# Kernel optimization log

Hardware: AMD Instinct MI355X
Metric: run time of the kernel (lower is better)

## Reference

```python
import jax, jax.numpy as jnp
import numpy as np

B, S, D, H = 64, 256, 2048, 16
HD = D // H

def setup_inputs() -> dict:
    key = jax.random.key(0)
    k1, k2, k3 = jax.random.split(key, 3)
    x = jax.random.normal(k1, (B, S, D), dtype=jnp.float32)
    # torch Linear weights: [out_features, in_features], scaled like kaiming-ish init
    w_qkv = jax.random.normal(k2, (3 * D, D), dtype=jnp.float32) * (1.0 / np.sqrt(D))
    w_o = jax.random.normal(k3, (D, D), dtype=jnp.float32) * (1.0 / np.sqrt(D))
    return {"x": x, "w_qkv": w_qkv, "w_o": w_o}

def reference(x, w_qkv, w_o):
    b, s, d = x.shape
    qkv = jnp.einsum('bsd,ed->bse', x, w_qkv)            # [B,S,3D]
    qkv = qkv.reshape(b, s, 3, H, HD).transpose(2, 0, 3, 1, 4)  # [3,B,H,S,HD]
    q, k, v = qkv[0], qkv[1], qkv[2]
    scores = jnp.einsum('bhqd,bhkd->bhqk', q, k) * (HD ** -0.5)  # [B,H,S,S]
    causal = jnp.triu(jnp.ones((s, s), dtype=bool), 1)
    scores = jnp.where(causal, jnp.float32(-1e9), scores)
    a = jax.nn.softmax(scores, axis=-1)
    ctx = jnp.einsum('bhqk,bhkd->bhqd', a, v)            # [B,H,S,HD]
    ctx = ctx.transpose(0, 2, 1, 3).reshape(b, s, d)     # [B,S,D]
    return jnp.einsum('bsd,ed->bse', ctx, w_o)
```

## Files before the change

kernel.cpp:

```cpp
#include <hip/hip_runtime.h>

#define NB 64
#define NS 256
#define ND 2048
#define NH 16
#define NHD 128

typedef unsigned short ushort_t;
typedef __attribute__((ext_vector_type(8))) __bf16 bf16x8;
typedef __attribute__((ext_vector_type(4))) short shortx4;
typedef __attribute__((ext_vector_type(4))) float f32x4;
typedef __attribute__((ext_vector_type(4))) unsigned short ushortx4;

__device__ __forceinline__ unsigned short f2bf(float f) {
  union { float f; unsigned int u; } v; v.f = f;
  unsigned int r = v.u + 0x7FFFu + ((v.u >> 16) & 1u);
  return (unsigned short)(r >> 16);
}

__device__ __forceinline__ void gload16(const void* g, void* l) {
  __builtin_amdgcn_global_load_lds(
      (__attribute__((address_space(1))) void*)(void*)(g),
      (__attribute__((address_space(3))) void*)(l), 16, 0, 0);
}

__global__ void cast_f32_bf16(const float* __restrict__ in, ushort_t* __restrict__ out, long n) {
  long i = ((long)blockIdx.x * blockDim.x + threadIdx.x) * 4;
  if (i + 3 < n) {
    float4 v = *reinterpret_cast<const float4*>(in + i);
    ushortx4 o;
    o.x = f2bf(v.x); o.y = f2bf(v.y); o.z = f2bf(v.z); o.w = f2bf(v.w);
    *reinterpret_cast<ushortx4*>(out + i) = o;
  }
}

template<int MODE>
__global__ __launch_bounds__(512, 2) void gemm256(const ushort_t* __restrict__ A,
                                                  const ushort_t* __restrict__ Bt,
                                                  float* __restrict__ Cf,
                                                  ushort_t* __restrict__ Cq,
                                                  int M, int N, int K) {
  extern __shared__ char smem[];
  const int tid = threadIdx.x;
  const int wv = tid >> 6, lane = tid & 63;
  const int l15 = lane & 15, lg = lane >> 4;
  const int wm = wv >> 2, wn = wv & 3;

  const int nbn = N >> 8;
  const int nwg = (M >> 8) * nbn;
  const int bid = blockIdx.x;
  const int q8 = nwg >> 3, r8 = nwg & 7;
  const int xcd = bid & 7, lin = bid >> 3;
  const int wg = (xcd < r8 ? xcd * (q8 + 1) : r8 * (q8 + 1) + (xcd - r8) * q8) + lin;
  const int m0 = (wg / nbn) << 8;
  const int n0 = (wg % nbn) << 8;

  const int srow = wv * 16 + (lane >> 2);
  const int sce = ((lane & 3) * 8) ^ (((srow >> 1) & 3) << 3);
  const ushort_t* pa0 = A  + (long)(m0 + srow) * K + sce;
  const ushort_t* pa1 = pa0 + (long)128 * K;
  const ushort_t* pb0 = Bt + (long)(n0 + srow) * K + sce;
  const ushort_t* pb1 = pb0 + (long)128 * K;

  const int c = (lg * 16) ^ (((l15 >> 1) & 3) << 4);

  f32x4 acc[8][4] = {};
  const int nkt = K >> 5;

  bf16x8 faA[8], faB[4], fbA[8], fbB[4];

  #pragma unroll
  for (int tt = 0; tt < 3; ++tt) {
    char* d = smem + tt * 32768 + wv * 1024;
    const long ko = (long)tt * 32;
    gload16(pa0 + ko, d);
    gload16(pa1 + ko, d + 8192);
    gload16(pb0 + ko, d + 16384);
    gload16(pb1 + ko, d + 24576);
  }
  asm volatile("s_waitcnt vmcnt(8)" ::: "memory");
  __builtin_amdgcn_s_barrier();
  __builtin_amdgcn_sched_barrier(0);
  #pragma unroll
  for (int i = 0; i < 8; ++i)
    faA[i] = *reinterpret_cast<const bf16x8*>(smem + (wm * 128 + i * 16 + l15) * 64 + c);
  #pragma unroll
  for (int j = 0; j < 4; ++j)
    faB[j] = *reinterpret_cast<const bf16x8*>(smem + 16384 + (wn * 64 + j * 16 + l15) * 64 + c);
  asm volatile("s_waitcnt vmcnt(4)" ::: "memory");

#define TILE(T_, CA_, CB_, NA_, NB_)                                           \
  {                                                                            \
    const int t_ = (T_);                                                       \
    __builtin_amdgcn_s_barrier();                                              \
    asm volatile("s_waitcnt lgkmcnt(0)" ::: "memory");                         \
    __builtin_amdgcn_sched_barrier(0);                                         \
    __builtin_amdgcn_s_setprio(1);                                             \
    if (t_ + 1 < nkt) {                                                        \
      const char* rb = smem + ((t_ + 1) & 3) * 32768;                          \
      _Pragma("unroll")                                                        \
      for (int i = 0; i < 8; ++i)                                              \
        NA_[i] = *reinterpret_cast<const bf16x8*>(rb + (wm * 128 + i * 16 + l15) * 64 + c); \
      _Pragma("unroll")                                                        \
      for (int j = 0; j < 4; ++j)                                              \
        NB_[j] = *reinterpret_cast<const bf16x8*>(rb + 16384 + (wn * 64 + j * 16 + l15) * 64 + c); \
    }                                                                          \
    if (t_ + 3 < nkt) {                                                        \
      char* d = smem + ((t_ + 3) & 3) * 32768 + wv * 1024;                     \
      const long ko = (long)(t_ + 3) * 32;                                     \
      gload16(pa0 + ko, d);                                                    \
      gload16(pa1 + ko, d + 8192);                                             \
      gload16(pb0 + ko, d + 16384);                                            \
      gload16(pb1 + ko, d + 24576);                                            \
    }                                                                          \
    _Pragma("unroll")                                                          \
    for (int i = 0; i < 8; ++i)                                                \
      _Pragma("unroll")                                                        \
      for (int j = 0; j < 4; ++j)                                              \
        acc[i][j] = __builtin_amdgcn_mfma_f32_16x16x32_bf16(CA_[i], CB_[j], acc[i][j], 0, 0, 0); \
              \
    _Pragma("unroll")                                                          \
    for (int g = 0; g < 8; ++g) {                                              \
      __builtin_amdgcn_sched_group_barrier(0x008, 4, 0);                       \
      if (g < 6) __builtin_amdgcn_sched_group_barrier(0x100, 2, 0);            \
      if (g < 4) __builtin_amdgcn_sched_group_barrier(0x010, 1, 0);            \
    }                                                                          \
    __builtin_amdgcn_s_setprio(0);                                             \
    __builtin_amdgcn_sched_barrier(0);                                         \
    if (t_ + 3 < nkt) asm volatile("s_waitcnt vmcnt(4)" ::: "memory");         \
    else              asm volatile("s_waitcnt vmcnt(0)" ::: "memory");         \
  }

  for (int t = 0; t < nkt; t += 2) {
    TILE(t,     faA, faB, fbA, fbB);
    TILE(t + 1, fbA, fbB, faA, faB);
  }
#undef TILE

  #pragma unroll
  for (int k = 0; k < 8; ++k) {
    const int mrow = m0 + wm * 128 + k * 16 + lg * 4;
    #pragma unroll
    for (int j = 0; j < 4; ++j) {
      const int n = n0 + wn * 64 + j * 16 + l15;
      #pragma unroll
      for (int r = 0; r < 4; ++r) {
        const int m = mrow + r;
        const float v = acc[k][j][r];
        if (MODE == 0) {
          Cf[(long)m * N + n] = v;
        } else {
          const int tq = n >> 11, hh = (n >> 7) & 15, hd = n & 127;
          const int b = m >> 8, s = m & 255;
          Cq[((((long)tq * NB + b) * NH + hh) * NS + s) * NHD + hd] = f2bf(v);
        }
      }
    }
  }
}

__global__ __launch_bounds__(512) void attn_fused(const ushort_t* __restrict__ qkv,
                                                  ushort_t* __restrict__ ctx) {
  const int bh = blockIdx.x;
  const int b = bh >> 4, h = bh & 15;
  const int wave = threadIdx.x >> 6, lane = threadIdx.x & 63;
  const int l15 = lane & 15, lg = lane >> 4;
  const long head_off = ((long)(b * NH + h)) * (NS * NHD);
  const ushort_t* Qp = qkv + head_off;
  const ushort_t* Kp = qkv + (long)NB * NH * NS * NHD + head_off;
  const ushort_t* Vp = qkv + 2L * NB * NH * NS * NHD + head_off;
  const int q0 = wave * 32;

  bf16x8 qf[2][4];
  #pragma unroll
  for (int ni = 0; ni < 2; ++ni)
    #pragma unroll
    for (int kk = 0; kk < 4; ++kk)
      qf[ni][kk] = *reinterpret_cast<const bf16x8*>(Qp + (q0 + ni * 16 + l15) * NHD + kk * 32 + lg * 8);

  f32x4 o[8][2] = {};
  float mstate[2] = {-1e30f, -1e30f};
  float lstate[2] = {0.f, 0.f};
  const float scale = 0.08838834764831845f;
  const int ntiles = (q0 + 32 + 63) >> 6;

  for (int kt = 0; kt < ntiles; ++kt) {
    f32x4 st[4][2] = {};
    #pragma unroll
    for (int kk = 0; kk < 4; ++kk) {
      bf16x8 kf[4];
      #pragma unroll
      for (int mi = 0; mi < 4; ++mi)
        kf[mi] = *reinterpret_cast<const bf16x8*>(Kp + (kt * 64 + mi * 16 + l15) * NHD + kk * 32 + lg * 8);
      #pragma unroll
      for (int mi = 0; mi < 4; ++mi)
        #pragma unroll
        for (int ni = 0; ni < 2; ++ni)
          st[mi][ni] = __builtin_amdgcn_mfma_f32_16x16x32_bf16(kf[mi], qf[ni][kk], st[mi][ni], 0, 0, 0);
    }
    const bool last = (kt == ntiles - 1);
    #pragma unroll
    for (int mi = 0; mi < 4; ++mi)
      #pragma unroll
      for (int ni = 0; ni < 2; ++ni)
        #pragma unroll
        for (int r = 0; r < 4; ++r) {
          const int kc = kt * 64 + mi * 16 + lg * 4 + r;
          const int q = q0 + ni * 16 + l15;
          float v = st[mi][ni][r] * scale;
          if (last && kc > q) v = -1e30f;
          st[mi][ni][r] = v;
        }
    shortx4 p[4][2];
    #pragma unroll
    for (int ni = 0; ni < 2; ++ni) {
      float tmax = -1e30f;
      #pragma unroll
      for (int mi = 0; mi < 4; ++mi)
        #pragma unroll
        for (int r = 0; r < 4; ++r) tmax = fmaxf(tmax, st[mi][ni][r]);
      tmax = fmaxf(tmax, __shfl_xor(tmax, 16, 64));
      tmax = fmaxf(tmax, __shfl_xor(tmax, 32, 64));
      const float mnew = fmaxf(mstate[ni], tmax);
      const float alpha = __expf(mstate[ni] - mnew);
      float tsum = 0.f;
      #pragma unroll
      for (int mi = 0; mi < 4; ++mi)
        #pragma unroll
        for (int r = 0; r < 4; ++r) {
          const float pe = __expf(st[mi][ni][r] - mnew);
          st[mi][ni][r] = pe;
          tsum += pe;
        }
      tsum += __shfl_xor(tsum, 16, 64);
      tsum += __shfl_xor(tsum, 32, 64);
      lstate[ni] = lstate[ni] * alpha + tsum;
      mstate[ni] = mnew;
      #pragma unroll
      for (int f = 0; f < 8; ++f)
        #pragma unroll
        for (int r = 0; r < 4; ++r) o[f][ni][r] *= alpha;
      #pragma unroll
      for (int mi = 0; mi < 4; ++mi)
        #pragma unroll
        for (int r = 0; r < 4; ++r) p[mi][ni][r] = (short)f2bf(st[mi][ni][r]);
    }
    #pragma unroll
    for (int f = 0; f < 8; ++f)
      #pragma unroll
      for (int mi = 0; mi < 4; ++mi) {
        shortx4 vt;
        #pragma unroll
        for (int j = 0; j < 4; ++j)
          vt[j] = (short)Vp[(kt * 64 + mi * 16 + lg * 4 + j) * NHD + f * 16 + l15];
        #pragma unroll
        for (int ni = 0; ni < 2; ++ni)
          o[f][ni] = __builtin_amdgcn_mfma_f32_16x16x16bf16_1k(vt, p[mi][ni], o[f][ni], 0, 0, 0);
      }
  }
  const float inv0 = 1.f / lstate[0], inv1 = 1.f / lstate[1];
  #pragma unroll
  for (int f = 0; f < 8; ++f)
    #pragma unroll
    for (int ni = 0; ni < 2; ++ni) {
      const float inv = ni ? inv1 : inv0;
      const int q = q0 + ni * 16 + l15;
      const int hd = f * 16 + lg * 4;
      ushortx4 ov;
      #pragma unroll
      for (int r = 0; r < 4; ++r) ov[r] = f2bf(o[f][ni][r] * inv);
      *reinterpret_cast<ushortx4*>(ctx + ((long)(b * NS + q)) * ND + h * NHD + hd) = ov;
    }
}

extern "C" void kernel_launch(void* const* d_in, const int* in_sizes, int n_in,
                              void* d_out, int out_size, void* d_ws, size_t ws_size,
                              hipStream_t stream) {
  const float* x     = (const float*)d_in[0];
  const float* w_qkv = (const float*)d_in[1];
  const float* w_o   = (const float*)d_in[2];
  char* ws = (char*)d_ws;
  if (ws_size < 369098752UL) return;
  ushort_t* xb    = (ushort_t*)(ws);
  ushort_t* wqkvb = (ushort_t*)(ws + 67108864L);
  ushort_t* wob   = (ushort_t*)(ws + 92274688L);
  ushort_t* qkvb  = (ushort_t*)(ws + 100663296L);
  ushort_t* ctxb  = (ushort_t*)(ws + 301989888L);

  const long nx = (long)NB * NS * ND;
  const long nq = 3L * ND * ND;
  const long no = (long)ND * ND;
  cast_f32_bf16<<<dim3(nx / 1024), 256, 0, stream>>>(x, xb, nx);
  cast_f32_bf16<<<dim3(nq / 1024), 256, 0, stream>>>(w_qkv, wqkvb, nq);
  cast_f32_bf16<<<dim3(no / 1024), 256, 0, stream>>>(w_o, wob, no);

  const int lds_bytes = 4 * 32768;
  (void)hipFuncSetAttribute(reinterpret_cast<const void*>(&gemm256<1>),
                            hipFuncAttributeMaxDynamicSharedMemorySize, lds_bytes);
  (void)hipFuncSetAttribute(reinterpret_cast<const void*>(&gemm256<0>),
                            hipFuncAttributeMaxDynamicSharedMemorySize, lds_bytes);

  gemm256<1><<<dim3(64 * 24), 512, lds_bytes, stream>>>(xb, wqkvb, nullptr, qkvb,
                                                        NB * NS, 3 * ND, ND);
  attn_fused<<<dim3(NB * NH), 512, 0, stream>>>(qkvb, ctxb);
  gemm256<0><<<dim3(64 * 8), 512, lds_bytes, stream>>>(ctxb, wob, (float*)d_out, nullptr,
                                                       NB * NS, ND, ND);
}
```

Baseline: 705.8 us.

## Pre-transpose V and balance causal query blocks across waves

Adds a kernel that transposes V per head into [hd][s] layout, reusing the x bf16 buffer, so the PV MFMA operand becomes one vector load instead of four scattered scalar loads. The attention kernel also pairs each wave's 16 early query rows with 16 late rows, which balances causal work across waves and skips MFMAs for the early block once it is fully masked. The cost is an extra launch and a full read and write pass over V.

```diff
diff --git a/kernel.cpp b/kernel.cpp
--- a/kernel.cpp
+++ b/kernel.cpp
@@ -32,6 +32,19 @@
     o.x = f2bf(v.x); o.y = f2bf(v.y); o.z = f2bf(v.z); o.w = f2bf(v.w);
     *reinterpret_cast<ushortx4*>(out + i) = o;
   }
+}
+
+__global__ void transpose_v(const ushort_t* __restrict__ qkv_v, ushort_t* __restrict__ vt) {
+  const int g = blockIdx.x * 256 + threadIdx.x;
+  const int s = g & 255;
+  const int hd8 = (g >> 8) & 15;
+  const int bh = g >> 12;
+  const ushort_t* src = qkv_v + ((long)bh << 15) + s * 128 + hd8 * 8;
+  ushortx4 v0 = *reinterpret_cast<const ushortx4*>(src);
+  ushortx4 v1 = *reinterpret_cast<const ushortx4*>(src + 4);
+  ushort_t* dst = vt + ((long)bh << 15) + (long)(hd8 * 8) * 256 + s;
+  dst[0] = v0.x; dst[256] = v0.y; dst[512] = v0.z; dst[768] = v0.w;
+  dst[1024] = v1.x; dst[1280] = v1.y; dst[1536] = v1.z; dst[1792] = v1.w;
 }
 
 template<int MODE>
@@ -118,7 +131,6 @@
       _Pragma("unroll")                                                        \
       for (int j = 0; j < 4; ++j)                                              \
         acc[i][j] = __builtin_amdgcn_mfma_f32_16x16x32_bf16(CA_[i], CB_[j], acc[i][j], 0, 0, 0); \
-              \
     _Pragma("unroll")                                                          \
     for (int g = 0; g < 8; ++g) {                                              \
       __builtin_amdgcn_sched_group_barrier(0x008, 4, 0);                       \
@@ -160,6 +172,7 @@
 }
 
 __global__ __launch_bounds__(512) void attn_fused(const ushort_t* __restrict__ qkv,
+                                                  const ushort_t* __restrict__ vT,
                                                   ushort_t* __restrict__ ctx) {
   const int bh = blockIdx.x;
   const int b = bh >> 4, h = bh & 15;
@@ -168,23 +181,24 @@
   const long head_off = ((long)(b * NH + h)) * (NS * NHD);
   const ushort_t* Qp = qkv + head_off;
   const ushort_t* Kp = qkv + (long)NB * NH * NS * NHD + head_off;
-  const ushort_t* Vp = qkv + 2L * NB * NH * NS * NHD + head_off;
-  const int q0 = wave * 32;
+  const ushort_t* vTp = vT + ((long)bh << 15);
+  const int q0[2] = { wave * 16, 240 - wave * 16 };
+  const int klast[2] = { (wave * 16 + 15) >> 6, (255 - wave * 16) >> 6 };
 
   bf16x8 qf[2][4];
   #pragma unroll
   for (int ni = 0; ni < 2; ++ni)
     #pragma unroll
     for (int kk = 0; kk < 4; ++kk)
-      qf[ni][kk] = *reinterpret_cast<const bf16x8*>(Qp + (q0 + ni * 16 + l15) * NHD + kk * 32 + lg * 8);
+      qf[ni][kk] = *reinterpret_cast<const bf16x8*>(Qp + (q0[ni] + l15) * NHD + kk * 32 + lg * 8);
 
   f32x4 o[8][2] = {};
   float mstate[2] = {-1e30f, -1e30f};
   float lstate[2] = {0.f, 0.f};
   const float scale = 0.08838834764831845f;
-  const int ntiles = (q0 + 32 + 63) >> 6;
-
-  for (int kt = 0; kt < ntiles; ++kt) {
+
+  for (int kt = 0; kt <= klast[1]; ++kt) {
+    const bool act0 = (kt <= klast[0]);
     f32x4 st[4][2] = {};
     #pragma unroll
     for (int kk = 0; kk < 4; ++kk) {
@@ -193,27 +207,27 @@
       for (int mi = 0; mi < 4; ++mi)
         kf[mi] = *reinterpret_cast<const bf16x8*>(Kp + (kt * 64 + mi * 16 + l15) * NHD + kk * 32 + lg * 8);
       #pragma unroll
-      for (int mi = 0; mi < 4; ++mi)
-        #pragma unroll
-        for (int ni = 0; ni < 2; ++ni)
-          st[mi][ni] = __builtin_amdgcn_mfma_f32_16x16x32_bf16(kf[mi], qf[ni][kk], st[mi][ni], 0, 0, 0);
+      for (int mi = 0; mi < 4; ++mi) {
+        st[mi][1] = __builtin_amdgcn_mfma_f32_16x16x32_bf16(kf[mi], qf[1][kk], st[mi][1], 0, 0, 0);
+        if (act0)
+          st[mi][0] = __builtin_amdgcn_mfma_f32_16x16x32_bf16(kf[mi], qf[0][kk], st[mi][0], 0, 0, 0);
+      }
     }
-    const bool last = (kt == ntiles - 1);
-    #pragma unroll
-    for (int mi = 0; mi < 4; ++mi)
-      #pragma unroll
-      for (int ni = 0; ni < 2; ++ni)
+    shortx4 p[4][2];
+    #pragma unroll
+    for (int ni = 0; ni < 2; ++ni) {
+      if (ni == 0 && !act0) continue;
+      const bool dom = (kt == klast[ni]);
+      const int q = q0[ni] + l15;
+      #pragma unroll
+      for (int mi = 0; mi < 4; ++mi)
         #pragma unroll
         for (int r = 0; r < 4; ++r) {
           const int kc = kt * 64 + mi * 16 + lg * 4 + r;
-          const int q = q0 + ni * 16 + l15;
           float v = st[mi][ni][r] * scale;
-          if (last && kc > q) v = -1e30f;
+          if (dom && kc > q) v = -1e30f;
           st[mi][ni][r] = v;
         }
-    shortx4 p[4][2];
-    #pragma unroll
-    for (int ni = 0; ni < 2; ++ni) {
       float tmax = -1e30f;
       #pragma unroll
       for (int mi = 0; mi < 4; ++mi)
@@ -249,13 +263,11 @@
     for (int f = 0; f < 8; ++f)
       #pragma unroll
       for (int mi = 0; mi < 4; ++mi) {
-        shortx4 vt;
-        #pragma unroll
-        for (int j = 0; j < 4; ++j)
-          vt[j] = (short)Vp[(kt * 64 + mi * 16 + lg * 4 + j) * NHD + f * 16 + l15];
-        #pragma unroll
-        for (int ni = 0; ni < 2; ++ni)
-          o[f][ni] = __builtin_amdgcn_mfma_f32_16x16x16bf16_1k(vt, p[mi][ni], o[f][ni], 0, 0, 0);
+        const shortx4 vt4 = *reinterpret_cast<const shortx4*>(
+            vTp + (f * 16 + l15) * NS + kt * 64 + mi * 16 + lg * 4);
+        o[f][1] = __builtin_amdgcn_mfma_f32_16x16x16bf16_1k(vt4, p[mi][1], o[f][1], 0, 0, 0);
+        if (act0)
+          o[f][0] = __builtin_amdgcn_mfma_f32_16x16x16bf16_1k(vt4, p[mi][0], o[f][0], 0, 0, 0);
       }
   }
   const float inv0 = 1.f / lstate[0], inv1 = 1.f / lstate[1];
@@ -264,7 +276,7 @@
     #pragma unroll
     for (int ni = 0; ni < 2; ++ni) {
       const float inv = ni ? inv1 : inv0;
-      const int q = q0 + ni * 16 + l15;
+      const int q = q0[ni] + l15;
       const int hd = f * 16 + lg * 4;
       ushortx4 ov;
       #pragma unroll
@@ -286,6 +298,7 @@
   ushort_t* wob   = (ushort_t*)(ws + 92274688L);
   ushort_t* qkvb  = (ushort_t*)(ws + 100663296L);
   ushort_t* ctxb  = (ushort_t*)(ws + 301989888L);
+  ushort_t* vTb   = xb;
 
   const long nx = (long)NB * NS * ND;
   const long nq = 3L * ND * ND;
@@ -302,7 +315,8 @@
 
   gemm256<1><<<dim3(64 * 24), 512, lds_bytes, stream>>>(xb, wqkvb, nullptr, qkvb,
                                                         NB * NS, 3 * ND, ND);
-  attn_fused<<<dim3(NB * NH), 512, 0, stream>>>(qkvb, ctxb);
+  transpose_v<<<dim3(16384), 256, 0, stream>>>(qkvb + 2L * NB * NH * NS * NHD, vTb);
+  attn_fused<<<dim3(NB * NH), 512, 0, stream>>>(qkvb, vTb, ctxb);
   gemm256<0><<<dim3(64 * 8), 512, lds_bytes, stream>>>(ctxb, wob, (float*)d_out, nullptr,
                                                        NB * NS, ND, ND);
 }
```

Measured after the change: 854.1 us. 1.21x slower.
